# Optimization experiments

Measured on AMD Instinct MI355X. Metric: run time of the kernel, lower is better.

Reference implementation:

```python
import jax, jax.numpy as jnp
import numpy as np

B, T, C, HS = 4, 4096, 1024, 64  # batch, seq, n_embd, head_size


def setup_inputs() -> dict:
    key = jax.random.key(0)
    kx, kq, kk, kv = jax.random.split(key, 4)
    s = 1.0 / np.sqrt(C)  # Linear-like init scale
    return {
        "x": jax.random.normal(kx, (B, T, C), dtype=jnp.float32),
        "Wq": jax.random.normal(kq, (C, HS), dtype=jnp.float32) * s,
        "bq": jnp.zeros((HS,), dtype=jnp.float32),
        "Wk": jax.random.normal(kk, (C, HS), dtype=jnp.float32) * s,
        "bk": jnp.zeros((HS,), dtype=jnp.float32),
        "Wv": jax.random.normal(kv, (C, HS), dtype=jnp.float32) * s,
        "bv": jnp.zeros((HS,), dtype=jnp.float32),
    }


def reference(x, Wq, bq, Wk, bk, Wv, bv):
    # x: [B,T,C]
    q = x @ Wq + bq          # [B,T,HS]
    k = x @ Wk + bk          # [B,T,HS]
    v = x @ Wv + bv          # [B,T,HS]
    att = jnp.einsum("bqh,bkh->bqk", q, k)  # [B,T,T]
    att = att * (C ** -0.5)  # NOTE: scales by n_embd, not head_size (faithful to source)
    causal = jnp.tril(jnp.ones((T, T), dtype=bool))
    att = jnp.where(causal, att, -jnp.inf)
    att = jax.nn.softmax(att, axis=-1)
    # dropout p=0.0 (eval): identity
    out = jnp.einsum("bqk,bkh->bqh", att, v)  # [B,T,HS]
    return out
```

## Files before the change

### kernel.cpp

```cpp
#include <hip/hip_runtime.h>
#include <hip/hip_bf16.h>
#include <math.h>

#define B 4
#define T 4096
#define C 1024
#define HS 64

typedef __attribute__((ext_vector_type(8))) short short8;
typedef __attribute__((ext_vector_type(4))) float f32x4;
typedef __attribute__((ext_vector_type(16))) float f32x16;

#define MFMA16(a, b, c) __builtin_amdgcn_mfma_f32_16x16x32_bf16((a), (b), (c), 0, 0, 0)
#define MFMA32(a, b, c) __builtin_amdgcn_mfma_f32_32x32x16_bf16((a), (b), (c), 0, 0, 0)

#define QSCALE 0.0450842200278f

static __device__ __forceinline__ unsigned short f2bf(float f) {
  union { float f; unsigned u; } v; v.f = f;
  unsigned r = v.u + 0x7FFFu + ((v.u >> 16) & 1u);
  return (unsigned short)(r >> 16);
}

static __device__ __forceinline__ unsigned pack_bf2(float lo, float hi2) {
  union { __hip_bfloat16 h; unsigned short u; } a, c;
  a.h = __float2bfloat16(lo); c.h = __float2bfloat16(hi2);
  return (unsigned)a.u | ((unsigned)c.u << 16);
}

__global__ __launch_bounds__(256) void conv_w_kernel(
    const float* __restrict__ Wq, const float* __restrict__ Wk,
    const float* __restrict__ Wv, unsigned short* __restrict__ Wt) {
  const int wi = blockIdx.x >> 4;
  const int c0 = (blockIdx.x & 15) * 64;
  const float* W = (wi == 0) ? Wq : (wi == 1) ? Wk : Wv;
  __shared__ float ws[64][65];
  const int t = threadIdx.x;
  const int r = t >> 2;
  const int cb = (t & 3) * 16;
#pragma unroll
  for (int j = 0; j < 4; ++j) {
    const f32x4 v = *(const f32x4*)&W[(size_t)(c0 + r) * HS + cb + 4 * j];
    ws[cb + 4 * j + 0][r] = v[0];
    ws[cb + 4 * j + 1][r] = v[1];
    ws[cb + 4 * j + 2][r] = v[2];
    ws[cb + 4 * j + 3][r] = v[3];
  }
  __syncthreads();
  const int h = t >> 2;
  const int rb = (t & 3) * 16;
  union { short8 s8[2]; unsigned short u[16]; } o;
#pragma unroll
  for (int i = 0; i < 16; ++i) o.u[i] = f2bf(ws[h][rb + i]);
  short8* dst = (short8*)(Wt + (size_t)(wi * 64 + h) * C + c0 + rb);
  dst[0] = o.s8[0];
  dst[1] = o.s8[1];
}

__global__ __launch_bounds__(512, 2) void proj_kernel(
    const float* __restrict__ x, const unsigned short* __restrict__ Wt,
    const float* __restrict__ bq, const float* __restrict__ bk,
    const float* __restrict__ bv,
    unsigned short* __restrict__ Qf, unsigned short* __restrict__ Kf,
    unsigned short* __restrict__ Vf) {
  const int m0   = blockIdx.x * 64;
  const int w    = threadIdx.x >> 6;
  const int lane = threadIdx.x & 63;
  const int col  = lane & 15, grp = lane >> 4;
  const int wm   = w >> 2;
  const int wn   = w & 3;
  const int phase = blockIdx.x & 7;

  __shared__ unsigned short A_lds[2][64 * 128];
  __shared__ unsigned short B_lds[2][48][512];

  const int arow  = threadIdx.x >> 3;
  const int akoff = (threadIdx.x & 7) * 16;
  const float* xp = x + (size_t)(m0 + arow) * C + akoff;

  f32x4 acc[2][3];
#pragma unroll
  for (int mf = 0; mf < 2; ++mf)
#pragma unroll
    for (int jj = 0; jj < 3; ++jj) acc[mf][jj] = (f32x4){0.f, 0.f, 0.f, 0.f};

  auto kcOf = [&](int it) { return ((it + phase) & 7) * 128; };

  auto stageB = [&](int nb, int kc) {
#pragma unroll
    for (int j = 0; j < 6; ++j) {
      const int f   = w * 6 + j;
      const int nt  = f % 12;
      const int k32 = f / 12;
      const unsigned short* src =
          Wt + (size_t)(nt * 16 + col) * C + kc + k32 * 32 + grp * 8;
      __builtin_amdgcn_global_load_lds(
          (const __attribute__((address_space(1))) void*)src,
          (__attribute__((address_space(3))) void*)&B_lds[nb][f][0],
          16, 0, 0);
    }
  };

  auto loadAreg = [&](int kc, f32x4 (&r)[4]) {
#pragma unroll
    for (int i = 0; i < 4; ++i) r[i] = *(const f32x4*)(xp + kc + 4 * i);
  };

  auto writeA = [&](int nb, const f32x4 (&r)[4]) {
    union { short8 s8[2]; unsigned short u[16]; } o;
#pragma unroll
    for (int i = 0; i < 4; ++i)
#pragma unroll
      for (int e = 0; e < 4; ++e) o.u[4 * i + e] = f2bf(r[i][e]);
    const int b0 = arow * 256 + (threadIdx.x & 7) * 32;
    const int s  = (arow & 7) << 4;
    char* base = (char*)&A_lds[nb][0];
    *(short8*)(base + ((b0     ) ^ s)) = o.s8[0];
    *(short8*)(base + ((b0 + 16) ^ s)) = o.s8[1];
  };

  auto readA = [&](int buf, int mf, int k32) {
    const int row = wm * 32 + mf * 16 + col;
    const int b = row * 256 + ((k32 * 64 + grp * 16) ^ ((col & 7) << 4));
    return *(const short8*)((const char*)&A_lds[buf][0] + b);
  };

  auto compute = [&](int buf) {
#pragma unroll
    for (int k32 = 0; k32 < 4; ++k32) {
      const short8 a0 = readA(buf, 0, k32);
      const short8 a1 = readA(buf, 1, k32);
#pragma unroll
      for (int jj = 0; jj < 3; ++jj) {
        const short8 bf =
            *(const short8*)&B_lds[buf][k32 * 12 + wn * 3 + jj][(size_t)lane * 8];
        acc[0][jj] = MFMA16(a0, bf, acc[0][jj]);
        acc[1][jj] = MFMA16(a1, bf, acc[1][jj]);
      }
    }
  };

  f32x4 arA[4];
  loadAreg(kcOf(0), arA);
  stageB(0, kcOf(0));
  writeA(0, arA);
  loadAreg(kcOf(1), arA);
  __syncthreads();

  for (int it = 0; it < 8; ++it) {
    const int buf = it & 1;
    if (it < 7) stageB(buf ^ 1, kcOf(it + 1));
    compute(buf);
    if (it < 7) {
      writeA(buf ^ 1, arA);
      if (it < 6) loadAreg(kcOf(it + 2), arA);
    }
    __syncthreads();
  }

  auto writeOut = [&](int row, int n, float v) {
    const int bb  = row >> 12;
    const int t   = row & (T - 1);
    const int blk = t >> 5;
    const int r   = t & 31;
    if (n < 64) {
      const int j = n >> 4, h2 = (n >> 3) & 1, e = n & 7;
      Qf[((((size_t)bb * 128 + blk) * 4 + j) * 64 + h2 * 32 + r) * 8 + e] =
          f2bf(v * QSCALE);
    } else if (n < 128) {
      const int d = n - 64;
      const int f = d >> 4, h2 = (d >> 3) & 1, e = d & 7;
      Kf[((((size_t)bb * 128 + blk) * 4 + f) * 64 + h2 * 32 + r) * 8 + e] =
          f2bf(v);
    } else {
      const int d = n - 128;
      const int e = r & 7, h2 = (r >> 3) & 1, half = (r >> 4) & 1;
      const int vi = ((d >> 5) << 1) + half;
      const int q = d & 31;
      Vf[((((size_t)bb * 128 + blk) * 4 + vi) * 64 + h2 * 32 + q) * 8 + e] =
          f2bf(v);
    }
  };
#pragma unroll
  for (int mf = 0; mf < 2; ++mf) {
#pragma unroll
    for (int jj = 0; jj < 3; ++jj) {
      const int n = wn * 48 + jj * 16 + col;
      const float bias = (n < 64) ? bq[n] : (n < 128) ? bk[n - 64] : bv[n - 128];
#pragma unroll
      for (int r = 0; r < 4; ++r)
        writeOut(m0 + wm * 32 + mf * 16 + 4 * grp + r, n, acc[mf][jj][r] + bias);
    }
  }
}

__global__ __launch_bounds__(256, 2) void attn_kernel(
    const unsigned short* __restrict__ Qf,
    const unsigned short* __restrict__ Kf,
    const unsigned short* __restrict__ Vf,
    float* __restrict__ out) {
  const int x8 = blockIdx.x & 7;
  const int kk = blockIdx.x >> 3;
  const int b  = x8 >> 1;
  const int qt = (kk << 1) | (x8 & 1);

  const int lane = threadIdx.x & 63;
  const int w    = threadIdx.x >> 6;
  const int q    = lane & 31;
  const int hi   = lane >> 5;
  const int qbase = qt * 32;
  const int qg    = qbase + q;

  __shared__ float accL[4][64][33];
  __shared__ float lL[4][32], invL[32];

  const unsigned short* Qp = Qf + ((size_t)(b * 128 + qt) * 4) * 512;
  const unsigned short* Kb = Kf + ((size_t)b * 128) * 4 * 512;
  const unsigned short* Vb = Vf + ((size_t)b * 128) * 4 * 512;

  short8 qf[4];
#pragma unroll
  for (int j = 0; j < 4; ++j)
    qf[j] = *(const short8*)(Qp + j * 512 + lane * 8);

  f32x16 acc0, acc1;
#pragma unroll
  for (int r = 0; r < 16; ++r) { acc0[r] = 0.f; acc1[r] = 0.f; }
  float lsum = 0.f;

  const int nkv = qt + 1;

  short8 kA[4], vA[4], kB[4], vB[4];

  auto loadKV = [&](int kb, short8 (&kd)[4], short8 (&vd)[4]) {
    const unsigned short* p = Kb + (size_t)kb * 2048 + lane * 8;
    kd[0] = *(const short8*)(p);
    kd[1] = *(const short8*)(p + 512);
    kd[2] = *(const short8*)(p + 1024);
    kd[3] = *(const short8*)(p + 1536);
    const unsigned short* vp = Vb + (size_t)kb * 2048 + lane * 8;
    vd[0] = *(const short8*)(vp);
    vd[1] = *(const short8*)(vp + 512);
    vd[2] = *(const short8*)(vp + 1024);
    vd[3] = *(const short8*)(vp + 1536);
  };

  auto step = [&](int kb, short8 (&kc)[4], short8 (&vc)[4],
                  short8 (&kn)[4], short8 (&vn)[4]) {
    int knb = kb + 4;
    if (knb > 127) knb = 127;
    loadKV(knb, kn, vn);

    f32x16 s;
#pragma unroll
    for (int r = 0; r < 16; ++r) s[r] = -8.0f;
    s = MFMA32(kc[0], qf[0], s);
    s = MFMA32(kc[1], qf[1], s);
    s = MFMA32(kc[2], qf[2], s);
    s = MFMA32(kc[3], qf[3], s);

    float pe[16];
    if (kb == qt) {
      const int qrel = qg - kb * 32;
#pragma unroll
      for (int r = 0; r < 16; ++r) {
        const int key = (r & 3) + 8 * (r >> 2) + 4 * hi;
        const float v = exp2f(s[r]);
        pe[r] = (key <= qrel) ? v : 0.f;
      }
    } else {
#pragma unroll
      for (int r = 0; r < 16; ++r) pe[r] = exp2f(s[r]);
    }
#pragma unroll
    for (int r = 0; r < 16; ++r) lsum += pe[r];

    unsigned own[8], oth[8];
#pragma unroll
    for (int j = 0; j < 8; ++j) own[j] = pack_bf2(pe[2 * j], pe[2 * j + 1]);
#pragma unroll
    for (int j = 0; j < 8; ++j) oth[j] = __shfl_xor(own[j], 32, 64);
    union U { short8 s8; unsigned u[4]; };
    U p0, p1;
    p0.u[0] = hi ? oth[2] : own[0];
    p0.u[1] = hi ? oth[3] : own[1];
    p0.u[2] = hi ? own[2] : oth[0];
    p0.u[3] = hi ? own[3] : oth[1];
    p1.u[0] = hi ? oth[6] : own[4];
    p1.u[1] = hi ? oth[7] : own[5];
    p1.u[2] = hi ? own[6] : oth[4];
    p1.u[3] = hi ? own[7] : oth[5];

    acc0 = MFMA32(vc[0], p0.s8, acc0);
    acc0 = MFMA32(vc[1], p1.s8, acc0);
    acc1 = MFMA32(vc[2], p0.s8, acc1);
    acc1 = MFMA32(vc[3], p1.s8, acc1);
  };

  if (w < nkv) {
    loadKV(w, kA, vA);
    int kb = w;
    while (true) {
      step(kb, kA, vA, kB, vB); kb += 4; if (kb >= nkv) break;
      step(kb, kB, vB, kA, vA); kb += 4; if (kb >= nkv) break;
    }
  }

  lsum += __shfl_xor(lsum, 32, 64);
  if (hi == 0) lL[w][q] = lsum;
#pragma unroll
  for (int r = 0; r < 16; ++r) {
    const int d = (r & 3) + 8 * (r >> 2) + 4 * hi;
    accL[w][d][q]      = acc0[r];
    accL[w][d + 32][q] = acc1[r];
  }
  __syncthreads();
  if (threadIdx.x < 32) {
    const int qq = threadIdx.x;
    const float L = lL[0][qq] + lL[1][qq] + lL[2][qq] + lL[3][qq];
    invL[qq] = 1.f / L;
  }
  __syncthreads();
#pragma unroll
  for (int p = 0; p < 8; ++p) {
    const int qq = (threadIdx.x >> 6) + 4 * p;
    const int d  = threadIdx.x & 63;
    const float v = accL[0][d][qq] + accL[1][d][qq] +
                    accL[2][d][qq] + accL[3][d][qq];
    out[(size_t)(b * T + qbase + qq) * HS + d] = v * invL[qq];
  }
}

extern "C" void kernel_launch(void* const* d_in, const int* in_sizes, int n_in,
                              void* d_out, int out_size, void* d_ws, size_t ws_size,
                              hipStream_t stream) {
  const float* x  = (const float*)d_in[0];
  const float* Wq = (const float*)d_in[1];
  const float* bq = (const float*)d_in[2];
  const float* Wk = (const float*)d_in[3];
  const float* bk = (const float*)d_in[4];
  const float* Wv = (const float*)d_in[5];
  const float* bv = (const float*)d_in[6];
  float* out = (float*)d_out;

  unsigned short* Qf = (unsigned short*)d_ws;
  unsigned short* Kf = Qf + (size_t)B * T * HS;
  unsigned short* Vf = Kf + (size_t)B * T * HS;
  unsigned short* Wt = Vf + (size_t)B * T * HS;

  conv_w_kernel<<<48, 256, 0, stream>>>(Wq, Wk, Wv, Wt);
  proj_kernel<<<B * T / 64, 512, 0, stream>>>(x, Wt, bq, bk, bv, Qf, Kf, Vf);
  attn_kernel<<<B * (T / 32), 256, 0, stream>>>(Qf, Kf, Vf, out);
}
```

Measured before the change: 59.43 us.

## Pair complementary causal query tiles per block for load balance

Each attention block now has 8 waves split into two groups. One group processes query tile p and the other processes tile 127-p, so every block carries equal causal work. The grid shrinks to one block per pair of tiles. The LDS reduction buffers double in size, which may limit how many blocks fit on one CU.

New measurement: 55.54 us. -6.5%, faster.

```diff
diff --git a/kernel.cpp b/kernel.cpp
--- a/kernel.cpp
+++ b/kernel.cpp
@@ -194,25 +194,27 @@
   }
 }
 
-__global__ __launch_bounds__(256, 2) void attn_kernel(
+__global__ __launch_bounds__(512, 2) void attn_kernel(
     const unsigned short* __restrict__ Qf,
     const unsigned short* __restrict__ Kf,
     const unsigned short* __restrict__ Vf,
     float* __restrict__ out) {
   const int x8 = blockIdx.x & 7;
-  const int kk = blockIdx.x >> 3;
   const int b  = x8 >> 1;
-  const int qt = (kk << 1) | (x8 & 1);
-
+  const int p  = ((blockIdx.x >> 3) << 1) | (x8 & 1);
+
+  const int w8   = threadIdx.x >> 6;
+  const int g    = w8 >> 2;
+  const int w    = w8 & 3;
   const int lane = threadIdx.x & 63;
-  const int w    = threadIdx.x >> 6;
   const int q    = lane & 31;
   const int hi   = lane >> 5;
+  const int qt   = g ? (127 - p) : p;
   const int qbase = qt * 32;
   const int qg    = qbase + q;
 
-  __shared__ float accL[4][64][33];
-  __shared__ float lL[4][32], invL[32];
+  __shared__ float accL[8][64][33];
+  __shared__ float lL[8][32], invL[2][32];
 
   const unsigned short* Qp = Qf + ((size_t)(b * 128 + qt) * 4) * 512;
   const unsigned short* Kb = Kf + ((size_t)b * 128) * 4 * 512;
@@ -233,16 +235,16 @@
   short8 kA[4], vA[4], kB[4], vB[4];
 
   auto loadKV = [&](int kb, short8 (&kd)[4], short8 (&vd)[4]) {
-    const unsigned short* p = Kb + (size_t)kb * 2048 + lane * 8;
-    kd[0] = *(const short8*)(p);
-    kd[1] = *(const short8*)(p + 512);
-    kd[2] = *(const short8*)(p + 1024);
-    kd[3] = *(const short8*)(p + 1536);
-    const unsigned short* vp = Vb + (size_t)kb * 2048 + lane * 8;
-    vd[0] = *(const short8*)(vp);
-    vd[1] = *(const short8*)(vp + 512);
-    vd[2] = *(const short8*)(vp + 1024);
-    vd[3] = *(const short8*)(vp + 1536);
+    const unsigned short* pk = Kb + (size_t)kb * 2048 + lane * 8;
+    kd[0] = *(const short8*)(pk);
+    kd[1] = *(const short8*)(pk + 512);
+    kd[2] = *(const short8*)(pk + 1024);
+    kd[3] = *(const short8*)(pk + 1536);
+    const unsigned short* pv = Vb + (size_t)kb * 2048 + lane * 8;
+    vd[0] = *(const short8*)(pv);
+    vd[1] = *(const short8*)(pv + 512);
+    vd[2] = *(const short8*)(pv + 1024);
+    vd[3] = *(const short8*)(pv + 1536);
   };
 
   auto step = [&](int kb, short8 (&kc)[4], short8 (&vc)[4],
@@ -307,27 +309,32 @@
   }
 
   lsum += __shfl_xor(lsum, 32, 64);
-  if (hi == 0) lL[w][q] = lsum;
+  if (hi == 0) lL[w8][q] = lsum;
 #pragma unroll
   for (int r = 0; r < 16; ++r) {
     const int d = (r & 3) + 8 * (r >> 2) + 4 * hi;
-    accL[w][d][q]      = acc0[r];
-    accL[w][d + 32][q] = acc1[r];
+    accL[w8][d][q]      = acc0[r];
+    accL[w8][d + 32][q] = acc1[r];
   }
   __syncthreads();
-  if (threadIdx.x < 32) {
-    const int qq = threadIdx.x;
-    const float L = lL[0][qq] + lL[1][qq] + lL[2][qq] + lL[3][qq];
-    invL[qq] = 1.f / L;
+  if (threadIdx.x < 64) {
+    const int g2 = threadIdx.x >> 5;
+    const int qq = threadIdx.x & 31;
+    const float L = lL[g2 * 4 + 0][qq] + lL[g2 * 4 + 1][qq] +
+                    lL[g2 * 4 + 2][qq] + lL[g2 * 4 + 3][qq];
+    invL[g2][qq] = 1.f / L;
   }
   __syncthreads();
-#pragma unroll
-  for (int p = 0; p < 8; ++p) {
-    const int qq = (threadIdx.x >> 6) + 4 * p;
-    const int d  = threadIdx.x & 63;
-    const float v = accL[0][d][qq] + accL[1][d][qq] +
-                    accL[2][d][qq] + accL[3][d][qq];
-    out[(size_t)(b * T + qbase + qq) * HS + d] = v * invL[qq];
+  {
+    const int tid2 = threadIdx.x & 255;
+#pragma unroll
+    for (int pp = 0; pp < 8; ++pp) {
+      const int qq = (tid2 >> 6) + 4 * pp;
+      const int d  = tid2 & 63;
+      const float v = accL[g * 4 + 0][d][qq] + accL[g * 4 + 1][d][qq] +
+                      accL[g * 4 + 2][d][qq] + accL[g * 4 + 3][d][qq];
+      out[(size_t)(b * T + qbase + qq) * HS + d] = v * invL[g][qq];
+    }
   }
 }
 
@@ -350,5 +357,5 @@
 
   conv_w_kernel<<<48, 256, 0, stream>>>(Wq, Wk, Wv, Wt);
   proj_kernel<<<B * T / 64, 512, 0, stream>>>(x, Wt, bq, bk, bv, Qf, Kf, Vf);
-  attn_kernel<<<B * (T / 32), 256, 0, stream>>>(Qf, Kf, Vf, out);
-}
+  attn_kernel<<<B * 64, 512, 0, stream>>>(Qf, Kf, Vf, out);
+}
```
